# Performance work log

Measured on AMD Instinct MI355X. Metric: run time of the kernel, lower is better.

## Reference

```python
import jax, jax.numpy as jnp
import numpy as np

N = 50000
IN_C = 128
HID = 64
HEADS = 4
OUT_C = 64
E_RAND = 800000
NEG_SLOPE = 0.2  # PyG GATConv default


def setup_inputs() -> dict:
    key = jax.random.key(0)
    ks = jax.random.split(key, 10)
    x = jax.random.normal(ks[0], (N, IN_C), dtype=jnp.float32)
    src = jax.random.randint(ks[1], (E_RAND,), 0, N)
    dst = jax.random.randint(ks[2], (E_RAND,), 0, N)
    loops = jnp.arange(N)
    # PyG GATConv adds self-loops by default; append them here
    edge_index = jnp.stack([jnp.concatenate([src, loops]),
                            jnp.concatenate([dst, loops])], axis=0).astype(jnp.int64)
    s = 0.05
    W1 = jax.random.normal(ks[3], (IN_C, HEADS * HID), dtype=jnp.float32) * s
    att_src1 = jax.random.normal(ks[4], (HEADS, HID), dtype=jnp.float32) * s
    att_dst1 = jax.random.normal(ks[5], (HEADS, HID), dtype=jnp.float32) * s
    b1 = jnp.zeros((HEADS * HID,), dtype=jnp.float32)
    W2 = jax.random.normal(ks[6], (HEADS * HID, OUT_C), dtype=jnp.float32) * s
    att_src2 = jax.random.normal(ks[7], (1, OUT_C), dtype=jnp.float32) * s
    att_dst2 = jax.random.normal(ks[8], (1, OUT_C), dtype=jnp.float32) * s
    b2 = jnp.zeros((OUT_C,), dtype=jnp.float32)
    return {"x": x, "edge_index": edge_index, "W1": W1, "att_src1": att_src1,
            "att_dst1": att_dst1, "b1": b1, "W2": W2, "att_src2": att_src2,
            "att_dst2": att_dst2, "b2": b2}


def gat_conv(x, src, dst, W, att_src, att_dst, bias, heads, ch, concat):
    n = x.shape[0]
    h = (x @ W).reshape(n, heads, ch)                      # [N,H,C]
    a_src = jnp.einsum('nhc,hc->nh', h, att_src)           # [N,H]
    a_dst = jnp.einsum('nhc,hc->nh', h, att_dst)
    e = jax.nn.leaky_relu(a_src[src] + a_dst[dst], NEG_SLOPE)  # [E,H]
    # segment softmax over incoming edges of each dst node
    m = jax.ops.segment_max(e, dst, num_segments=n)
    ex = jnp.exp(e - m[dst])
    ssum = jax.ops.segment_sum(ex, dst, num_segments=n)
    alpha = ex / jnp.where(ssum[dst] > 0, ssum[dst], 1.0)  # [E,H]
    msg = h[src] * alpha[:, :, None]                        # [E,H,C]
    out = jax.ops.segment_sum(msg, dst, num_segments=n)     # [N,H,C]
    out = out.reshape(n, heads * ch) if concat else out.mean(axis=1)
    return out + bias


def reference(x, edge_index, W1, att_src1, att_dst1, b1, W2, att_src2, att_dst2, b2):
    src, dst = edge_index[0], edge_index[1]
    # eval mode: feature dropout and attention dropout are identity
    h = gat_conv(x, src, dst, W1, att_src1, att_dst1, b1, HEADS, HID, True)
    h = jax.nn.elu(h)
    out = gat_conv(h, src, dst, W2, att_src2, att_dst2, b2, 1, OUT_C, False)
    return out
```

## Files before the change

### kernel.cpp

```cpp
#include <hip/hip_runtime.h>
#include <hip/hip_bf16.h>

#define IN_C 128
#define HID 64
#define HEADS 4
#define OUT_C 64
#define NEG_SLOPE 0.2f

typedef __attribute__((ext_vector_type(8))) short bfrag8;
typedef __attribute__((ext_vector_type(4))) float facc4;

__device__ __forceinline__ float bf16u_to_f(unsigned short u) {
  return __uint_as_float(((unsigned)u) << 16);
}

__global__ __launch_bounds__(256) void cvt_bf16_kernel(
    const float* __restrict__ in, unsigned short* __restrict__ out, int n8) {
  int i = blockIdx.x * blockDim.x + threadIdx.x;
  if (i >= n8) return;
  float4 v0 = *reinterpret_cast<const float4*>(&in[(size_t)i * 8]);
  float4 v1 = *reinterpret_cast<const float4*>(&in[(size_t)i * 8 + 4]);
  unsigned short q[8];
  q[0] = __bfloat16_as_ushort(__float2bfloat16(v0.x));
  q[1] = __bfloat16_as_ushort(__float2bfloat16(v0.y));
  q[2] = __bfloat16_as_ushort(__float2bfloat16(v0.z));
  q[3] = __bfloat16_as_ushort(__float2bfloat16(v0.w));
  q[4] = __bfloat16_as_ushort(__float2bfloat16(v1.x));
  q[5] = __bfloat16_as_ushort(__float2bfloat16(v1.y));
  q[6] = __bfloat16_as_ushort(__float2bfloat16(v1.z));
  q[7] = __bfloat16_as_ushort(__float2bfloat16(v1.w));
  *reinterpret_cast<uint4*>(&out[(size_t)i * 8]) =
      *reinterpret_cast<const uint4*>(q);
}

template <int HEADS_T>
__global__ __launch_bounds__(256) void mfma_gemm_attn(
    const unsigned short* __restrict__ A, const float* __restrict__ B,
    const float* __restrict__ att_src, const float* __restrict__ att_dst,
    unsigned short* __restrict__ Hout, float* __restrict__ a_src,
    float* __restrict__ a_dst, int M, int N, int K) {
  __shared__ unsigned short As[64 * 64];
  __shared__ unsigned short Bs[64 * 64];
  const int t = threadIdx.x;
  const int wid = t >> 6, lane = t & 63;
  const int lg = lane >> 4, li = lane & 15;
  const int bm = blockIdx.x * 64, bn = blockIdx.y * 64;
  const int head = blockIdx.y;

  facc4 acc[4];
#pragma unroll
  for (int fn = 0; fn < 4; ++fn) acc[fn] = (facc4)(0.f);

  const int ktiles = K >> 6;
  for (int kt = 0; kt < ktiles; ++kt) {
#pragma unroll
    for (int p = 0; p < 2; ++p) {
      int flat = t + p * 256;
      int row = flat >> 3, g = flat & 7;
      int gr = bm + row;
      uint4 v = make_uint4(0, 0, 0, 0);
      if (gr < M)
        v = *reinterpret_cast<const uint4*>(&A[(size_t)gr * K + kt * 64 + g * 8]);
      *reinterpret_cast<uint4*>(&As[row * 64 + ((g ^ (row & 7)) << 3)]) = v;
    }
#pragma unroll
    for (int p = 0; p < 4; ++p) {
      int flat = t + p * 256;
      int n = flat & 63, kg = flat >> 6;
      unsigned short q[4];
#pragma unroll
      for (int i = 0; i < 4; ++i)
        q[i] = __bfloat16_as_ushort(__float2bfloat16(
            B[(size_t)(kt * 64 + kg * 4 + i) * N + bn + n]));
      int g = kg >> 1, half = kg & 1;
      *reinterpret_cast<ushort4*>(
          &Bs[n * 64 + ((g ^ (n & 7)) << 3) + half * 4]) =
          *reinterpret_cast<const ushort4*>(q);
    }
    __syncthreads();
#pragma unroll
    for (int ks = 0; ks < 2; ++ks) {
      int arow = wid * 16 + li;
      int gk = ks * 4 + lg;
      bfrag8 a = *reinterpret_cast<const bfrag8*>(
          &As[arow * 64 + ((gk ^ (arow & 7)) << 3)]);
#pragma unroll
      for (int fn = 0; fn < 4; ++fn) {
        int col = fn * 16 + li;
        bfrag8 b = *reinterpret_cast<const bfrag8*>(
            &Bs[col * 64 + ((gk ^ (col & 7)) << 3)]);
        acc[fn] =
            __builtin_amdgcn_mfma_f32_16x16x32_bf16(a, b, acc[fn], 0, 0, 0);
      }
    }
    __syncthreads();
  }

  float s_att[4], d_att[4];
#pragma unroll
  for (int fn = 0; fn < 4; ++fn) {
    s_att[fn] = att_src[head * 64 + fn * 16 + li];
    d_att[fn] = att_dst[head * 64 + fn * 16 + li];
  }
#pragma unroll
  for (int reg = 0; reg < 4; ++reg) {
    int row = bm + wid * 16 + lg * 4 + reg;
    float ps = 0.f, pd = 0.f;
#pragma unroll
    for (int fn = 0; fn < 4; ++fn) {
      float c = acc[fn][reg];
      ps += c * s_att[fn];
      pd += c * d_att[fn];
    }
#pragma unroll
    for (int m = 1; m < 16; m <<= 1) {
      ps += __shfl_xor(ps, m);
      pd += __shfl_xor(pd, m);
    }
    if (row < M) {
#pragma unroll
      for (int fn = 0; fn < 4; ++fn)
        Hout[(size_t)row * N + bn + fn * 16 + li] =
            __bfloat16_as_ushort(__float2bfloat16(acc[fn][reg]));
      if (li == 0) {
        a_src[(size_t)row * HEADS_T + head] = ps;
        a_dst[(size_t)row * HEADS_T + head] = pd;
      }
    }
  }
}

__global__ void hist_kernel(const int* __restrict__ dst, int E,
                            int* __restrict__ deg) {
  int e = blockIdx.x * blockDim.x + threadIdx.x;
  if (e < E) atomicAdd(&deg[dst[e]], 1);
}

__device__ __forceinline__ int pad4(int d) { return (d + 3) & ~3; }

__global__ __launch_bounds__(256) void scan_partial_kernel(
    const int* __restrict__ deg, int n, int* __restrict__ partials) {
  __shared__ int sm[256];
  int t = threadIdx.x;
  int i = blockIdx.x * 256 + t;
  sm[t] = (i < n) ? pad4(deg[i]) : 0;
  __syncthreads();
  for (int off = 128; off > 0; off >>= 1) {
    if (t < off) sm[t] += sm[t + off];
    __syncthreads();
  }
  if (t == 0) partials[blockIdx.x] = sm[0];
}

__global__ __launch_bounds__(256) void scan_base_kernel(
    const int* __restrict__ partials, int nb, int* __restrict__ base) {
  __shared__ int sm[256];
  int t = threadIdx.x;
  int v = (t < nb) ? partials[t] : 0;
  sm[t] = v;
  __syncthreads();
  for (int off = 1; off < 256; off <<= 1) {
    int u = (t >= off) ? sm[t - off] : 0;
    __syncthreads();
    sm[t] += u;
    __syncthreads();
  }
  if (t < nb) base[t] = sm[t] - v;
}

__global__ __launch_bounds__(256) void scan_expand_kernel(
    const int* __restrict__ deg, int n, const int* __restrict__ base,
    int* __restrict__ offsets, int* __restrict__ cursor) {
  __shared__ int sm[256];
  int t = threadIdx.x;
  int i = blockIdx.x * 256 + t;
  int v = (i < n) ? pad4(deg[i]) : 0;
  sm[t] = v;
  __syncthreads();
  for (int off = 1; off < 256; off <<= 1) {
    int u = (t >= off) ? sm[t - off] : 0;
    __syncthreads();
    sm[t] += u;
    __syncthreads();
  }
  int excl = sm[t] - v + base[blockIdx.x];
  if (i < n) {
    offsets[i] = excl;
    cursor[i] = excl;
  }
}

__global__ void scatter_kernel(const int* __restrict__ src,
                               const int* __restrict__ dst, int E,
                               int* __restrict__ cursor,
                               int2* __restrict__ sedge) {
  int e = blockIdx.x * blockDim.x + threadIdx.x;
  if (e < E) {
    int d = dst[e];
    int pos = atomicAdd(&cursor[d], 1);
    sedge[pos] = make_int2(src[e], d);
  }
}

__global__ __launch_bounds__(256) void edge_p1_kernel(
    const int2* __restrict__ sedge, const float* __restrict__ as1,
    const float* __restrict__ ad1, float* __restrict__ p1,
    int* __restrict__ ssrc_c, int stride) {
  int i = blockIdx.x * blockDim.x + threadIdx.x;
  if (i >= stride) return;
  int2 e = sedge[i];
  bool valid = e.x >= 0;
  int s = valid ? e.x : 0;
  int d = valid ? e.y : 0;
  float4 a4 = *reinterpret_cast<const float4*>(&as1[s * 4]);
  float4 b4 = *reinterpret_cast<const float4*>(&ad1[d * 4]);
  float v[4] = {a4.x + b4.x, a4.y + b4.y, a4.z + b4.z, a4.w + b4.w};
#pragma unroll
  for (int h = 0; h < 4; ++h) {
    float x = v[h];
    x = (x > 0.f) ? x : NEG_SLOPE * x;
    float p = __expf(x);
    p1[(size_t)h * stride + i] = valid ? p : 0.f;
  }
  ssrc_c[i] = s;
}

__global__ __launch_bounds__(256) void edge_p2_kernel(
    const int2* __restrict__ sedge, const float* __restrict__ as2,
    const float* __restrict__ ad2, float* __restrict__ p2, int stride) {
  int i = blockIdx.x * blockDim.x + threadIdx.x;
  if (i >= stride) return;
  int2 e = sedge[i];
  bool valid = e.x >= 0;
  int s = valid ? e.x : 0;
  int d = valid ? e.y : 0;
  float x = as2[s] + ad2[d];
  x = (x > 0.f) ? x : NEG_SLOPE * x;
  float p = __expf(x);
  p2[i] = valid ? p : 0.f;
}

__global__ __launch_bounds__(256) void agg1_kernel(
    const unsigned short* __restrict__ h1, const float* __restrict__ p1,
    const int* __restrict__ ssrc_c, const int* __restrict__ offsets,
    const int* __restrict__ deg, const float* __restrict__ bias,
    unsigned short* __restrict__ out, int n_nodes, int stride) {
  int wave = (int)((blockIdx.x * blockDim.x + threadIdx.x) >> 6);
  int lane = threadIdx.x & 63;
  if (wave >= n_nodes) return;
  int head = lane >> 4;
  int off = offsets[wave];
  int cnt = deg[wave];
  int g4 = (cnt + 3) >> 2;
  int last = g4 - 1;
  const int* S_ = ssrc_c + off;
  const float* P_ = p1 + (size_t)head * stride + off;

  auto ldS = [&](int g) {
    return *reinterpret_cast<const int4*>(S_ + min(g, last) * 4);
  };
  auto ldP = [&](int g) {
    return *reinterpret_cast<const float4*>(P_ + min(g, last) * 4);
  };
  auto gat = [&](int s) {
    return *reinterpret_cast<const ushort4*>(&h1[(size_t)s * 256 + lane * 4]);
  };

  int4 S0 = ldS(0), S1 = ldS(1), S2 = ldS(2);
  float4 P0 = ldP(0), P1 = ldP(1);
  ushort4 H0 = gat(S0.x), H1 = gat(S0.y), H2 = gat(S0.z), H3 = gat(S0.w);
  ushort4 H4 = gat(S1.x), H5 = gat(S1.y), H6 = gat(S1.z), H7 = gat(S1.w);

  float l = 0.f, a0 = 0.f, a1 = 0.f, a2 = 0.f, a3 = 0.f;
  for (int j = 0; j <= last; ++j) {
    int4 S3 = ldS(j + 3);
    float4 P2 = ldP(j + 2);
    l += P0.x + P0.y + P0.z + P0.w;
    a0 += P0.x * bf16u_to_f(H0.x) + P0.y * bf16u_to_f(H1.x) +
          P0.z * bf16u_to_f(H2.x) + P0.w * bf16u_to_f(H3.x);
    a1 += P0.x * bf16u_to_f(H0.y) + P0.y * bf16u_to_f(H1.y) +
          P0.z * bf16u_to_f(H2.y) + P0.w * bf16u_to_f(H3.y);
    a2 += P0.x * bf16u_to_f(H0.z) + P0.y * bf16u_to_f(H1.z) +
          P0.z * bf16u_to_f(H2.z) + P0.w * bf16u_to_f(H3.z);
    a3 += P0.x * bf16u_to_f(H0.w) + P0.y * bf16u_to_f(H1.w) +
          P0.z * bf16u_to_f(H2.w) + P0.w * bf16u_to_f(H3.w);
    H0 = H4; H1 = H5; H2 = H6; H3 = H7;
    H4 = gat(S2.x); H5 = gat(S2.y); H6 = gat(S2.z); H7 = gat(S2.w);
    S0 = S1; S1 = S2; S2 = S3;
    P0 = P1; P1 = P2;
  }
  float inv = 1.0f / l;
  int col = lane * 4;
  float4 b4 = *reinterpret_cast<const float4*>(&bias[col]);
  float o0 = a0 * inv + b4.x;
  float o1 = a1 * inv + b4.y;
  float o2 = a2 * inv + b4.z;
  float o3 = a3 * inv + b4.w;
  o0 = o0 > 0.f ? o0 : __expf(o0) - 1.f;
  o1 = o1 > 0.f ? o1 : __expf(o1) - 1.f;
  o2 = o2 > 0.f ? o2 : __expf(o2) - 1.f;
  o3 = o3 > 0.f ? o3 : __expf(o3) - 1.f;
  unsigned short q[4];
  q[0] = __bfloat16_as_ushort(__float2bfloat16(o0));
  q[1] = __bfloat16_as_ushort(__float2bfloat16(o1));
  q[2] = __bfloat16_as_ushort(__float2bfloat16(o2));
  q[3] = __bfloat16_as_ushort(__float2bfloat16(o3));
  *reinterpret_cast<ushort4*>(&out[(size_t)wave * 256 + col]) =
      *reinterpret_cast<const ushort4*>(q);
}

__global__ __launch_bounds__(256) void agg2_kernel(
    const unsigned short* __restrict__ h2, const float* __restrict__ p2,
    const int* __restrict__ ssrc_c, const int* __restrict__ offsets,
    const int* __restrict__ deg, const float* __restrict__ bias,
    float* __restrict__ out, int n_nodes) {
  int wave = (int)((blockIdx.x * blockDim.x + threadIdx.x) >> 6);
  int lane = threadIdx.x & 63;
  if (wave >= n_nodes) return;
  int off = offsets[wave];
  int cnt = deg[wave];
  int g4 = (cnt + 3) >> 2;
  int last = g4 - 1;
  const int* S_ = ssrc_c + off;
  const float* P_ = p2 + off;

  auto ldS = [&](int g) {
    return *reinterpret_cast<const int4*>(S_ + min(g, last) * 4);
  };
  auto ldP = [&](int g) {
    return *reinterpret_cast<const float4*>(P_ + min(g, last) * 4);
  };
  auto gat = [&](int s) { return h2[(size_t)s * 64 + lane]; };

  int4 S0 = ldS(0), S1 = ldS(1), S2 = ldS(2);
  float4 P0 = ldP(0), P1 = ldP(1);
  unsigned short H0 = gat(S0.x), H1 = gat(S0.y), H2 = gat(S0.z), H3 = gat(S0.w);
  unsigned short H4 = gat(S1.x), H5 = gat(S1.y), H6 = gat(S1.z), H7 = gat(S1.w);

  float l = 0.f, acc = 0.f;
  for (int j = 0; j <= last; ++j) {
    int4 S3 = ldS(j + 3);
    float4 P2 = ldP(j + 2);
    l += P0.x + P0.y + P0.z + P0.w;
    acc += P0.x * bf16u_to_f(H0) + P0.y * bf16u_to_f(H1) +
           P0.z * bf16u_to_f(H2) + P0.w * bf16u_to_f(H3);
    H0 = H4; H1 = H5; H2 = H6; H3 = H7;
    H4 = gat(S2.x); H5 = gat(S2.y); H6 = gat(S2.z); H7 = gat(S2.w);
    S0 = S1; S1 = S2; S2 = S3;
    P0 = P1; P1 = P2;
  }
  out[(size_t)wave * 64 + lane] = acc / l + bias[lane];
}

extern "C" void kernel_launch(void* const* d_in, const int* in_sizes, int n_in,
                              void* d_out, int out_size, void* d_ws,
                              size_t ws_size, hipStream_t stream) {
  const float* x = (const float*)d_in[0];
  const int* edge_index = (const int*)d_in[1];
  const float* W1 = (const float*)d_in[2];
  const float* att_src1 = (const float*)d_in[3];
  const float* att_dst1 = (const float*)d_in[4];
  const float* b1 = (const float*)d_in[5];
  const float* W2 = (const float*)d_in[6];
  const float* att_src2 = (const float*)d_in[7];
  const float* att_dst2 = (const float*)d_in[8];
  const float* b2 = (const float*)d_in[9];

  const int n = in_sizes[0] / IN_C;
  const int E = in_sizes[1] / 2;
  const int* src = edge_index;
  const int* dst = edge_index + E;
  const int nb = (n + 255) / 256;
  const int stride = (E + 4 * n + 3) & ~3;

  char* ws = (char*)d_ws;
  size_t off = 0;
  auto carve = [&](size_t bytes) -> void* {
    void* p = ws + off;
    off = (off + bytes + 255) & ~(size_t)255;
    return p;
  };
  unsigned short* xb = (unsigned short*)carve((size_t)n * IN_C * 2);
  unsigned short* h1b = (unsigned short*)carve((size_t)n * 256 * 2);
  unsigned short* hact = (unsigned short*)carve((size_t)n * 256 * 2);
  unsigned short* h2b = (unsigned short*)carve((size_t)n * 64 * 2);
  float* as1 = (float*)carve((size_t)n * 4 * 4);
  float* ad1 = (float*)carve((size_t)n * 4 * 4);
  float* as2 = (float*)carve((size_t)n * 4);
  float* ad2 = (float*)carve((size_t)n * 4);
  int* deg = (int*)carve((size_t)n * 4);
  int* offsets = (int*)carve((size_t)n * 4);
  int* cursor = (int*)carve((size_t)n * 4);
  int2* sedge = (int2*)carve((size_t)stride * 8);
  int* ssrc_c = (int*)carve((size_t)stride * 4);
  float* p1 = (float*)carve((size_t)stride * 4 * 4);
  float* p2 = (float*)carve((size_t)stride * 4);
  int* partials = (int*)carve((size_t)nb * 4);
  int* base = (int*)carve((size_t)nb * 4);

  hipMemsetAsync(deg, 0, (size_t)n * 4, stream);
  hipMemsetAsync(sedge, 0xFF, (size_t)stride * 8, stream);

  {
    int n8 = n * IN_C / 8;
    cvt_bf16_kernel<<<(n8 + 255) / 256, 256, 0, stream>>>(x, xb, n8);
  }
  {
    dim3 g((n + 63) / 64, (HEADS * HID) / 64);
    mfma_gemm_attn<HEADS><<<g, 256, 0, stream>>>(
        xb, W1, att_src1, att_dst1, h1b, as1, ad1, n, HEADS * HID, IN_C);
  }
  hist_kernel<<<(E + 255) / 256, 256, 0, stream>>>(dst, E, deg);
  scan_partial_kernel<<<nb, 256, 0, stream>>>(deg, n, partials);
  scan_base_kernel<<<1, 256, 0, stream>>>(partials, nb, base);
  scan_expand_kernel<<<nb, 256, 0, stream>>>(deg, n, base, offsets, cursor);
  scatter_kernel<<<(E + 255) / 256, 256, 0, stream>>>(src, dst, E, cursor,
                                                      sedge);
  edge_p1_kernel<<<(stride + 255) / 256, 256, 0, stream>>>(sedge, as1, ad1, p1,
                                                           ssrc_c, stride);
  agg1_kernel<<<(n * 64 + 255) / 256, 256, 0, stream>>>(
      h1b, p1, ssrc_c, offsets, deg, b1, hact, n, stride);
  {
    dim3 g((n + 63) / 64, OUT_C / 64);
    mfma_gemm_attn<1><<<g, 256, 0, stream>>>(
        hact, W2, att_src2, att_dst2, h2b, as2, ad2, n, OUT_C, HEADS * HID);
  }
  edge_p2_kernel<<<(stride + 255) / 256, 256, 0, stream>>>(sedge, as2, ad2, p2,
                                                           stride);
  agg2_kernel<<<(n * 64 + 255) / 256, 256, 0, stream>>>(
      h2b, p2, ssrc_c, offsets, deg, b2, (float*)d_out, n);
}
```

Before: 330.7 us.

## Widen layer-1 GEMM, fuse scan stages, fold edge_p2 into agg2, deepen gather prefetch

Layer-1 GEMM now computes all 256 output columns per block, so the A tile is loaded once instead of once per head. The single-block scan_base kernel is merged into scan_expand, with each block redoing the small partials scan. edge_p2 is removed and agg2 computes the layer-2 attention exponentials inline from sedge. Both aggregation kernels get a deeper gather prefetch pipeline. This trades fewer launches and less intermediate traffic for more registers and LDS per block, and more index reads in agg2.

```diff
diff --git a/kernel.cpp b/kernel.cpp
--- a/kernel.cpp
+++ b/kernel.cpp
@@ -12,6 +12,9 @@
 
 __device__ __forceinline__ float bf16u_to_f(unsigned short u) {
   return __uint_as_float(((unsigned)u) << 16);
+}
+__device__ __forceinline__ unsigned short f_to_bf16u(float f) {
+  return __bfloat16_as_ushort(__float2bfloat16(f));
 }
 
 __global__ __launch_bounds__(256) void cvt_bf16_kernel(
@@ -21,20 +24,105 @@
   float4 v0 = *reinterpret_cast<const float4*>(&in[(size_t)i * 8]);
   float4 v1 = *reinterpret_cast<const float4*>(&in[(size_t)i * 8 + 4]);
   unsigned short q[8];
-  q[0] = __bfloat16_as_ushort(__float2bfloat16(v0.x));
-  q[1] = __bfloat16_as_ushort(__float2bfloat16(v0.y));
-  q[2] = __bfloat16_as_ushort(__float2bfloat16(v0.z));
-  q[3] = __bfloat16_as_ushort(__float2bfloat16(v0.w));
-  q[4] = __bfloat16_as_ushort(__float2bfloat16(v1.x));
-  q[5] = __bfloat16_as_ushort(__float2bfloat16(v1.y));
-  q[6] = __bfloat16_as_ushort(__float2bfloat16(v1.z));
-  q[7] = __bfloat16_as_ushort(__float2bfloat16(v1.w));
+  q[0] = f_to_bf16u(v0.x); q[1] = f_to_bf16u(v0.y);
+  q[2] = f_to_bf16u(v0.z); q[3] = f_to_bf16u(v0.w);
+  q[4] = f_to_bf16u(v1.x); q[5] = f_to_bf16u(v1.y);
+  q[6] = f_to_bf16u(v1.z); q[7] = f_to_bf16u(v1.w);
   *reinterpret_cast<uint4*>(&out[(size_t)i * 8]) =
       *reinterpret_cast<const uint4*>(q);
 }
 
-template <int HEADS_T>
-__global__ __launch_bounds__(256) void mfma_gemm_attn(
+__global__ __launch_bounds__(256) void mfma_gemm1_wide(
+    const unsigned short* __restrict__ A, const float* __restrict__ B,
+    const float* __restrict__ att_src, const float* __restrict__ att_dst,
+    unsigned short* __restrict__ Hout, float* __restrict__ a_src,
+    float* __restrict__ a_dst, int M) {
+  __shared__ unsigned short As[64 * 64];
+  __shared__ unsigned short Bs[256 * 64];
+  const int t = threadIdx.x;
+  const int wid = t >> 6, lane = t & 63;
+  const int lg = lane >> 4, li = lane & 15;
+  const int bm = blockIdx.x * 64;
+
+  facc4 acc[16];
+#pragma unroll
+  for (int fn = 0; fn < 16; ++fn) acc[fn] = (facc4)(0.f);
+
+#pragma unroll
+  for (int kt = 0; kt < 2; ++kt) {
+#pragma unroll
+    for (int p = 0; p < 2; ++p) {
+      int flat = t + p * 256;
+      int row = flat >> 3, g = flat & 7;
+      int gr = bm + row;
+      uint4 v = make_uint4(0, 0, 0, 0);
+      if (gr < M)
+        v = *reinterpret_cast<const uint4*>(&A[(size_t)gr * 128 + kt * 64 + g * 8]);
+      *reinterpret_cast<uint4*>(&As[row * 64 + ((g ^ (row & 7)) << 3)]) = v;
+    }
+#pragma unroll
+    for (int p = 0; p < 16; ++p) {
+      int n = t;
+      int kg = p;
+      unsigned short q[4];
+#pragma unroll
+      for (int i = 0; i < 4; ++i)
+        q[i] = f_to_bf16u(B[(size_t)(kt * 64 + kg * 4 + i) * 256 + n]);
+      int g = kg >> 1, half = kg & 1;
+      *reinterpret_cast<ushort4*>(&Bs[n * 64 + ((g ^ (n & 7)) << 3) + half * 4]) =
+          *reinterpret_cast<const ushort4*>(q);
+    }
+    __syncthreads();
+#pragma unroll
+    for (int ks = 0; ks < 2; ++ks) {
+      int arow = wid * 16 + li;
+      int gk = ks * 4 + lg;
+      bfrag8 a = *reinterpret_cast<const bfrag8*>(
+          &As[arow * 64 + ((gk ^ (arow & 7)) << 3)]);
+#pragma unroll
+      for (int fn = 0; fn < 16; ++fn) {
+        int col = fn * 16 + li;
+        bfrag8 b = *reinterpret_cast<const bfrag8*>(
+            &Bs[col * 64 + ((gk ^ (col & 7)) << 3)]);
+        acc[fn] =
+            __builtin_amdgcn_mfma_f32_16x16x32_bf16(a, b, acc[fn], 0, 0, 0);
+      }
+    }
+    __syncthreads();
+  }
+
+#pragma unroll
+  for (int reg = 0; reg < 4; ++reg) {
+    int row = bm + wid * 16 + lg * 4 + reg;
+    if (row < M) {
+#pragma unroll
+      for (int fn = 0; fn < 16; ++fn)
+        Hout[(size_t)row * 256 + fn * 16 + li] = f_to_bf16u(acc[fn][reg]);
+    }
+#pragma unroll
+    for (int h = 0; h < 4; ++h) {
+      float ps = 0.f, pd = 0.f;
+#pragma unroll
+      for (int q = 0; q < 4; ++q) {
+        int fn = h * 4 + q;
+        float c = acc[fn][reg];
+        ps += c * att_src[fn * 16 + li];
+        pd += c * att_dst[fn * 16 + li];
+      }
+#pragma unroll
+      for (int m = 1; m < 16; m <<= 1) {
+        ps += __shfl_xor(ps, m);
+        pd += __shfl_xor(pd, m);
+      }
+      if (row < M && li == 0) {
+        a_src[(size_t)row * 4 + h] = ps;
+        a_dst[(size_t)row * 4 + h] = pd;
+      }
+    }
+  }
+}
+
+__global__ __launch_bounds__(256) void mfma_gemm2(
     const unsigned short* __restrict__ A, const float* __restrict__ B,
     const float* __restrict__ att_src, const float* __restrict__ att_dst,
     unsigned short* __restrict__ Hout, float* __restrict__ a_src,
@@ -44,8 +132,7 @@
   const int t = threadIdx.x;
   const int wid = t >> 6, lane = t & 63;
   const int lg = lane >> 4, li = lane & 15;
-  const int bm = blockIdx.x * 64, bn = blockIdx.y * 64;
-  const int head = blockIdx.y;
+  const int bm = blockIdx.x * 64, bn = 0;
 
   facc4 acc[4];
 #pragma unroll
@@ -70,11 +157,9 @@
       unsigned short q[4];
 #pragma unroll
       for (int i = 0; i < 4; ++i)
-        q[i] = __bfloat16_as_ushort(__float2bfloat16(
-            B[(size_t)(kt * 64 + kg * 4 + i) * N + bn + n]));
+        q[i] = f_to_bf16u(B[(size_t)(kt * 64 + kg * 4 + i) * N + bn + n]);
       int g = kg >> 1, half = kg & 1;
-      *reinterpret_cast<ushort4*>(
-          &Bs[n * 64 + ((g ^ (n & 7)) << 3) + half * 4]) =
+      *reinterpret_cast<ushort4*>(&Bs[n * 64 + ((g ^ (n & 7)) << 3) + half * 4]) =
           *reinterpret_cast<const ushort4*>(q);
     }
     __syncthreads();
@@ -99,8 +184,8 @@
   float s_att[4], d_att[4];
 #pragma unroll
   for (int fn = 0; fn < 4; ++fn) {
-    s_att[fn] = att_src[head * 64 + fn * 16 + li];
-    d_att[fn] = att_dst[head * 64 + fn * 16 + li];
+    s_att[fn] = att_src[fn * 16 + li];
+    d_att[fn] = att_dst[fn * 16 + li];
   }
 #pragma unroll
   for (int reg = 0; reg < 4; ++reg) {
@@ -120,11 +205,10 @@
     if (row < M) {
 #pragma unroll
       for (int fn = 0; fn < 4; ++fn)
-        Hout[(size_t)row * N + bn + fn * 16 + li] =
-            __bfloat16_as_ushort(__float2bfloat16(acc[fn][reg]));
+        Hout[(size_t)row * N + bn + fn * 16 + li] = f_to_bf16u(acc[fn][reg]);
       if (li == 0) {
-        a_src[(size_t)row * HEADS_T + head] = ps;
-        a_dst[(size_t)row * HEADS_T + head] = pd;
+        a_src[row] = ps;
+        a_dst[row] = pd;
       }
     }
   }
@@ -152,27 +236,21 @@
   if (t == 0) partials[blockIdx.x] = sm[0];
 }
 
-__global__ __launch_bounds__(256) void scan_base_kernel(
-    const int* __restrict__ partials, int nb, int* __restrict__ base) {
+__global__ __launch_bounds__(256) void scan_expand_kernel(
+    const int* __restrict__ deg, int n, const int* __restrict__ partials,
+    int nb, int* __restrict__ offsets, int* __restrict__ cursor) {
+  __shared__ int smp[256];
   __shared__ int sm[256];
   int t = threadIdx.x;
-  int v = (t < nb) ? partials[t] : 0;
-  sm[t] = v;
+  smp[t] = (t < nb) ? partials[t] : 0;
   __syncthreads();
   for (int off = 1; off < 256; off <<= 1) {
-    int u = (t >= off) ? sm[t - off] : 0;
-    __syncthreads();
-    sm[t] += u;
-    __syncthreads();
-  }
-  if (t < nb) base[t] = sm[t] - v;
-}
-
-__global__ __launch_bounds__(256) void scan_expand_kernel(
-    const int* __restrict__ deg, int n, const int* __restrict__ base,
-    int* __restrict__ offsets, int* __restrict__ cursor) {
-  __shared__ int sm[256];
-  int t = threadIdx.x;
+    int u = (t >= off) ? smp[t - off] : 0;
+    __syncthreads();
+    smp[t] += u;
+    __syncthreads();
+  }
+  int base = (blockIdx.x > 0) ? smp[blockIdx.x - 1] : 0;
   int i = blockIdx.x * 256 + t;
   int v = (i < n) ? pad4(deg[i]) : 0;
   sm[t] = v;
@@ -183,7 +261,7 @@
     sm[t] += u;
     __syncthreads();
   }
-  int excl = sm[t] - v + base[blockIdx.x];
+  int excl = sm[t] - v + base;
   if (i < n) {
     offsets[i] = excl;
     cursor[i] = excl;
@@ -225,21 +303,6 @@
   ssrc_c[i] = s;
 }
 
-__global__ __launch_bounds__(256) void edge_p2_kernel(
-    const int2* __restrict__ sedge, const float* __restrict__ as2,
-    const float* __restrict__ ad2, float* __restrict__ p2, int stride) {
-  int i = blockIdx.x * blockDim.x + threadIdx.x;
-  if (i >= stride) return;
-  int2 e = sedge[i];
-  bool valid = e.x >= 0;
-  int s = valid ? e.x : 0;
-  int d = valid ? e.y : 0;
-  float x = as2[s] + ad2[d];
-  x = (x > 0.f) ? x : NEG_SLOPE * x;
-  float p = __expf(x);
-  p2[i] = valid ? p : 0.f;
-}
-
 __global__ __launch_bounds__(256) void agg1_kernel(
     const unsigned short* __restrict__ h1, const float* __restrict__ p1,
     const int* __restrict__ ssrc_c, const int* __restrict__ offsets,
@@ -251,8 +314,7 @@
   int head = lane >> 4;
   int off = offsets[wave];
   int cnt = deg[wave];
-  int g4 = (cnt + 3) >> 2;
-  int last = g4 - 1;
+  int last = ((cnt + 3) >> 2) - 1;
   const int* S_ = ssrc_c + off;
   const float* P_ = p1 + (size_t)head * stride + off;
 
@@ -266,15 +328,18 @@
     return *reinterpret_cast<const ushort4*>(&h1[(size_t)s * 256 + lane * 4]);
   };
 
-  int4 S0 = ldS(0), S1 = ldS(1), S2 = ldS(2);
-  float4 P0 = ldP(0), P1 = ldP(1);
-  ushort4 H0 = gat(S0.x), H1 = gat(S0.y), H2 = gat(S0.z), H3 = gat(S0.w);
-  ushort4 H4 = gat(S1.x), H5 = gat(S1.y), H6 = gat(S1.z), H7 = gat(S1.w);
+  int4 Sg;
+  ushort4 H0, H1, H2, H3, H4, H5, H6, H7, H8, H9, H10, H11;
+  Sg = ldS(0); H0 = gat(Sg.x); H1 = gat(Sg.y); H2 = gat(Sg.z); H3 = gat(Sg.w);
+  Sg = ldS(1); H4 = gat(Sg.x); H5 = gat(Sg.y); H6 = gat(Sg.z); H7 = gat(Sg.w);
+  Sg = ldS(2); H8 = gat(Sg.x); H9 = gat(Sg.y); H10 = gat(Sg.z); H11 = gat(Sg.w);
+  int4 S3 = ldS(3);
+  float4 P0 = ldP(0), P1v = ldP(1), P2v = ldP(2);
 
   float l = 0.f, a0 = 0.f, a1 = 0.f, a2 = 0.f, a3 = 0.f;
   for (int j = 0; j <= last; ++j) {
-    int4 S3 = ldS(j + 3);
-    float4 P2 = ldP(j + 2);
+    int4 S4 = ldS(j + 4);
+    float4 P3v = ldP(j + 3);
     l += P0.x + P0.y + P0.z + P0.w;
     a0 += P0.x * bf16u_to_f(H0.x) + P0.y * bf16u_to_f(H1.x) +
           P0.z * bf16u_to_f(H2.x) + P0.w * bf16u_to_f(H3.x);
@@ -285,9 +350,10 @@
     a3 += P0.x * bf16u_to_f(H0.w) + P0.y * bf16u_to_f(H1.w) +
           P0.z * bf16u_to_f(H2.w) + P0.w * bf16u_to_f(H3.w);
     H0 = H4; H1 = H5; H2 = H6; H3 = H7;
-    H4 = gat(S2.x); H5 = gat(S2.y); H6 = gat(S2.z); H7 = gat(S2.w);
-    S0 = S1; S1 = S2; S2 = S3;
-    P0 = P1; P1 = P2;
+    H4 = H8; H5 = H9; H6 = H10; H7 = H11;
+    H8 = gat(S3.x); H9 = gat(S3.y); H10 = gat(S3.z); H11 = gat(S3.w);
+    S3 = S4;
+    P0 = P1v; P1v = P2v; P2v = P3v;
   }
   float inv = 1.0f / l;
   int col = lane * 4;
@@ -301,53 +367,73 @@
   o2 = o2 > 0.f ? o2 : __expf(o2) - 1.f;
   o3 = o3 > 0.f ? o3 : __expf(o3) - 1.f;
   unsigned short q[4];
-  q[0] = __bfloat16_as_ushort(__float2bfloat16(o0));
-  q[1] = __bfloat16_as_ushort(__float2bfloat16(o1));
-  q[2] = __bfloat16_as_ushort(__float2bfloat16(o2));
-  q[3] = __bfloat16_as_ushort(__float2bfloat16(o3));
+  q[0] = f_to_bf16u(o0); q[1] = f_to_bf16u(o1);
+  q[2] = f_to_bf16u(o2); q[3] = f_to_bf16u(o3);
   *reinterpret_cast<ushort4*>(&out[(size_t)wave * 256 + col]) =
       *reinterpret_cast<const ushort4*>(q);
 }
 
 __global__ __launch_bounds__(256) void agg2_kernel(
-    const unsigned short* __restrict__ h2, const float* __restrict__ p2,
-    const int* __restrict__ ssrc_c, const int* __restrict__ offsets,
-    const int* __restrict__ deg, const float* __restrict__ bias,
-    float* __restrict__ out, int n_nodes) {
+    const unsigned short* __restrict__ h2, const float* __restrict__ as2,
+    const float* __restrict__ ad2, const int2* __restrict__ sedge,
+    const int* __restrict__ offsets, const int* __restrict__ deg,
+    const float* __restrict__ bias, float* __restrict__ out, int n_nodes) {
   int wave = (int)((blockIdx.x * blockDim.x + threadIdx.x) >> 6);
   int lane = threadIdx.x & 63;
   if (wave >= n_nodes) return;
   int off = offsets[wave];
   int cnt = deg[wave];
-  int g4 = (cnt + 3) >> 2;
-  int last = g4 - 1;
-  const int* S_ = ssrc_c + off;
-  const float* P_ = p2 + off;
+  int last = ((cnt + 3) >> 2) - 1;
+  const int2* E_ = sedge + off;
+  float ad = ad2[wave];
 
   auto ldS = [&](int g) {
-    return *reinterpret_cast<const int4*>(S_ + min(g, last) * 4);
-  };
-  auto ldP = [&](int g) {
-    return *reinterpret_cast<const float4*>(P_ + min(g, last) * 4);
-  };
-  auto gat = [&](int s) { return h2[(size_t)s * 64 + lane]; };
-
-  int4 S0 = ldS(0), S1 = ldS(1), S2 = ldS(2);
-  float4 P0 = ldP(0), P1 = ldP(1);
+    g = min(g, last);
+    int4 a = *reinterpret_cast<const int4*>(E_ + g * 4);
+    int4 b = *reinterpret_cast<const int4*>(E_ + g * 4 + 2);
+    return make_int4(a.x, a.z, b.x, b.z);
+  };
+  auto gAS = [&](int4 s) {
+    return make_float4(as2[max(s.x, 0)], as2[max(s.y, 0)], as2[max(s.z, 0)],
+                       as2[max(s.w, 0)]);
+  };
+  auto mkP = [&](int4 s, float4 a) {
+    float4 p;
+    float e;
+    e = a.x + ad; e = (e > 0.f) ? e : NEG_SLOPE * e;
+    p.x = (s.x >= 0) ? __expf(e) : 0.f;
+    e = a.y + ad; e = (e > 0.f) ? e : NEG_SLOPE * e;
+    p.y = (s.y >= 0) ? __expf(e) : 0.f;
+    e = a.z + ad; e = (e > 0.f) ? e : NEG_SLOPE * e;
+    p.z = (s.z >= 0) ? __expf(e) : 0.f;
+    e = a.w + ad; e = (e > 0.f) ? e : NEG_SLOPE * e;
+    p.w = (s.w >= 0) ? __expf(e) : 0.f;
+    return p;
+  };
+  auto gat = [&](int s) { return h2[(size_t)max(s, 0) * 64 + lane]; };
+
+  int4 S0 = ldS(0), S1 = ldS(1), S2 = ldS(2), S3 = ldS(3);
   unsigned short H0 = gat(S0.x), H1 = gat(S0.y), H2 = gat(S0.z), H3 = gat(S0.w);
   unsigned short H4 = gat(S1.x), H5 = gat(S1.y), H6 = gat(S1.z), H7 = gat(S1.w);
+  unsigned short H8 = gat(S2.x), H9 = gat(S2.y), H10 = gat(S2.z),
+                 H11 = gat(S2.w);
+  float4 AS1 = gAS(S1), AS2 = gAS(S2);
+  float4 P0 = mkP(S0, gAS(S0)), P1v = mkP(S1, AS1);
 
   float l = 0.f, acc = 0.f;
   for (int j = 0; j <= last; ++j) {
-    int4 S3 = ldS(j + 3);
-    float4 P2 = ldP(j + 2);
+    int4 S4 = ldS(j + 4);
+    float4 AS3 = gAS(S3);
+    float4 P2v = mkP(S2, AS2);
     l += P0.x + P0.y + P0.z + P0.w;
     acc += P0.x * bf16u_to_f(H0) + P0.y * bf16u_to_f(H1) +
            P0.z * bf16u_to_f(H2) + P0.w * bf16u_to_f(H3);
     H0 = H4; H1 = H5; H2 = H6; H3 = H7;
-    H4 = gat(S2.x); H5 = gat(S2.y); H6 = gat(S2.z); H7 = gat(S2.w);
-    S0 = S1; S1 = S2; S2 = S3;
-    P0 = P1; P1 = P2;
+    H4 = H8; H5 = H9; H6 = H10; H7 = H11;
+    H8 = gat(S3.x); H9 = gat(S3.y); H10 = gat(S3.z); H11 = gat(S3.w);
+    S2 = S3; S3 = S4;
+    AS2 = AS3;
+    P0 = P1v; P1v = P2v;
   }
   out[(size_t)wave * 64 + lane] = acc / l + bias[lane];
 }
@@ -394,9 +480,7 @@
   int2* sedge = (int2*)carve((size_t)stride * 8);
   int* ssrc_c = (int*)carve((size_t)stride * 4);
   float* p1 = (float*)carve((size_t)stride * 4 * 4);
-  float* p2 = (float*)carve((size_t)stride * 4);
   int* partials = (int*)carve((size_t)nb * 4);
-  int* base = (int*)carve((size_t)nb * 4);
 
   hipMemsetAsync(deg, 0, (size_t)n * 4, stream);
   hipMemsetAsync(sedge, 0xFF, (size_t)stride * 8, stream);
@@ -405,28 +489,20 @@
     int n8 = n * IN_C / 8;
     cvt_bf16_kernel<<<(n8 + 255) / 256, 256, 0, stream>>>(x, xb, n8);
   }
-  {
-    dim3 g((n + 63) / 64, (HEADS * HID) / 64);
-    mfma_gemm_attn<HEADS><<<g, 256, 0, stream>>>(
-        xb, W1, att_src1, att_dst1, h1b, as1, ad1, n, HEADS * HID, IN_C);
-  }
+  mfma_gemm1_wide<<<(n + 63) / 64, 256, 0, stream>>>(
+      xb, W1, att_src1, att_dst1, h1b, as1, ad1, n);
   hist_kernel<<<(E + 255) / 256, 256, 0, stream>>>(dst, E, deg);
   scan_partial_kernel<<<nb, 256, 0, stream>>>(deg, n, partials);
-  scan_base_kernel<<<1, 256, 0, stream>>>(partials, nb, base);
-  scan_expand_kernel<<<nb, 256, 0, stream>>>(deg, n, base, offsets, cursor);
+  scan_expand_kernel<<<nb, 256, 0, stream>>>(deg, n, partials, nb, offsets,
+                                             cursor);
   scatter_kernel<<<(E + 255) / 256, 256, 0, stream>>>(src, dst, E, cursor,
                                                       sedge);
   edge_p1_kernel<<<(stride + 255) / 256, 256, 0, stream>>>(sedge, as1, ad1, p1,
                                                            ssrc_c, stride);
   agg1_kernel<<<(n * 64 + 255) / 256, 256, 0, stream>>>(
       h1b, p1, ssrc_c, offsets, deg, b1, hact, n, stride);
-  {
-    dim3 g((n + 63) / 64, OUT_C / 64);
-    mfma_gemm_attn<1><<<g, 256, 0, stream>>>(
-        hact, W2, att_src2, att_dst2, h2b, as2, ad2, n, OUT_C, HEADS * HID);
-  }
-  edge_p2_kernel<<<(stride + 255) / 256, 256, 0, stream>>>(sedge, as2, ad2, p2,
-                                                           stride);
+  mfma_gemm2<<<(n + 63) / 64, 256, 0, stream>>>(
+      hact, W2, att_src2, att_dst2, h2b, as2, ad2, n, OUT_C, HEADS * HID);
   agg2_kernel<<<(n * 64 + 255) / 256, 256, 0, stream>>>(
-      h2b, p2, ssrc_c, offsets, deg, b2, (float*)d_out, n);
-}
+      h2b, as2, ad2, sedge, offsets, deg, b2, (float*)d_out, n);
+}
```

Measured after the change: 339.1 us. 2.5% more time.
